# Performance work log

Measured on AMD Instinct MI355X. Metric: run time of the kernel, lower is better.

## Reference

```python
import jax, jax.numpy as jnp
import numpy as np

K = 3
PAD = 1


def _deform_conv(x, offset, weight, bias):
    """torchvision-style deform_conv2d (v1, no mask), stride=1, pad=1, dil=1.
    x: [B,C,H,W], offset: [B,2*K*K,H,W] ordered (dy,dx) per kernel pos (row-major).
    """
    B, C, H, W = x.shape
    K2 = K * K
    off = offset.reshape(B, K2, 2, H, W)
    dy, dx = off[:, :, 0], off[:, :, 1]
    ky = jnp.repeat(jnp.arange(K), K).astype(x.dtype)  # [K2] kernel row offsets
    kx = jnp.tile(jnp.arange(K), K).astype(x.dtype)    # [K2] kernel col offsets
    hh = jnp.arange(H, dtype=x.dtype)
    ww = jnp.arange(W, dtype=x.dtype)
    # sampling positions: [B,K2,H,W]
    py = hh[None, None, :, None] + ky[None, :, None, None] - PAD + dy
    px = ww[None, None, None, :] + kx[None, :, None, None] - PAD + dx
    y0f = jnp.floor(py)
    x0f = jnp.floor(px)
    wy = py - y0f
    wx = px - x0f
    y0 = y0f.astype(jnp.int32)
    x0 = x0f.astype(jnp.int32)
    xf = x.reshape(B, C, H * W)

    def corner(iy, ix, w):
        # zero padding outside the image: contribution masked to 0
        valid = (iy >= 0) & (iy < H) & (ix >= 0) & (ix < W)
        iyc = jnp.clip(iy, 0, H - 1)
        ixc = jnp.clip(ix, 0, W - 1)
        lin = (iyc * W + ixc).reshape(B, -1)                      # [B,K2*H*W]
        g = jnp.take_along_axis(xf, lin[:, None, :], axis=2)     # [B,C,K2*H*W]
        g = g.reshape(B, C, K2, H, W)
        wv = (w * valid.astype(x.dtype))[:, None]                # [B,1,K2,H,W]
        return g * wv

    val = (corner(y0, x0, (1 - wy) * (1 - wx))
           + corner(y0, x0 + 1, (1 - wy) * wx)
           + corner(y0 + 1, x0, wy * (1 - wx))
           + corner(y0 + 1, x0 + 1, wy * wx))                    # [B,C,K2,H,W]
    O = weight.shape[0]
    out = jnp.einsum('ock,bckhw->bohw', weight.reshape(O, C, K2), val)
    return out + bias[None, :, None, None]


def setup_inputs() -> dict:
    key = jax.random.key(0)
    k1, k2, k3, k4, k5 = jax.random.split(key, 5)
    B, C, O, H, W = 4, 64, 64, 128, 128
    fan = C * K * K
    x = jax.random.normal(k1, (B, C, H, W), dtype=jnp.float32)
    w_off = jax.random.normal(k2, (2 * K * K, C, K, K), dtype=jnp.float32) / np.sqrt(fan)
    b_off = jax.random.normal(k3, (2 * K * K,), dtype=jnp.float32) * 0.01
    w_dcn = jax.random.normal(k4, (O, C, K, K), dtype=jnp.float32) / np.sqrt(fan)
    b_dcn = jax.random.normal(k5, (O,), dtype=jnp.float32) * 0.01
    return {"x": x, "w_off": w_off, "b_off": b_off, "w_dcn": w_dcn, "b_dcn": b_dcn}


def reference(x, w_off, b_off, w_dcn, b_dcn):
    offset = jax.lax.conv_general_dilated(
        x, w_off, window_strides=(1, 1), padding=((PAD, PAD), (PAD, PAD)),
        dimension_numbers=('NCHW', 'OIHW', 'NCHW')) + b_off[None, :, None, None]
    return _deform_conv(x, offset, w_dcn, b_dcn)
```

## Files before the change

kernel.cpp:

```cpp
#include <hip/hip_runtime.h>
#include <hip/hip_fp16.h>

#define HH 128
#define WW 128
#define CC 64
#define OO 64
#define HWSZ (HH*WW)

typedef _Float16 f16x8 __attribute__((ext_vector_type(8)));
typedef float    f32x4 __attribute__((ext_vector_type(4)));

__device__ __forceinline__ unsigned short f2h(float f) {
    return __half_as_ushort(__float2half_rn(f));
}

__global__ __launch_bounds__(256) void prep_all(const float* __restrict__ x,
                                                const float* __restrict__ wd,
                                                const float* __restrict__ wo,
                                                unsigned short* __restrict__ xh,
                                                unsigned short* __restrict__ wdtf,
                                                unsigned short* __restrict__ wotf) {
    int t = threadIdx.x;
    if (blockIdx.z == 4) {
        int i = (blockIdx.y * 2 + blockIdx.x) * 256 + t;
        if (i < 36864) {
            int j = i & 7, l = (i >> 3) & 63, nt = (i >> 9) & 3, kcb = i >> 11;
            int k = kcb >> 1, cb = kcb & 1;
            int o = nt * 16 + (l & 15);
            int c = cb * 32 + ((l >> 4) & 3) * 8 + j;
            wdtf[i] = f2h(wd[(o * 64 + c) * 9 + k]);
        } else if (i < 36864 + 18432) {
            int jdx = i - 36864;
            int j = jdx & 7, l = (jdx >> 3) & 63, nt = (jdx >> 9) & 1, kcb = jdx >> 10;
            int k = kcb >> 1, cb = kcb & 1;
            int oc = nt * 16 + (l & 15);
            int c = cb * 32 + ((l >> 4) & 3) * 8 + j;
            wotf[jdx] = f2h(oc < 18 ? wo[(oc * 64 + c) * 9 + k] : 0.0f);
        }
        return;
    }
    __shared__ float tile[64 * 65];
    int w0 = blockIdx.x * 64, h = blockIdx.y, b = blockIdx.z;
    const float* xb = x + ((long)b * CC * HWSZ) + h * WW + w0;
#pragma unroll
    for (int i = 0; i < 16; ++i) {
        int idx = i * 256 + t; int c = idx >> 6, w = idx & 63;
        tile[c * 65 + w] = xb[c * HWSZ + w];
    }
    __syncthreads();
    unsigned short* xo = xh + ((long)((b * HH + h) * WW + w0)) * CC;
#pragma unroll
    for (int i = 0; i < 8; ++i) {
        int idx = i * 256 + t; int w = idx >> 5, c = (idx & 31) * 2;
        ushort2 u;
        u.x = f2h(tile[c * 65 + w]);
        u.y = f2h(tile[(c + 1) * 65 + w]);
        *(ushort2*)(xo + w * CC + c) = u;
    }
}

__global__ __launch_bounds__(256, 2) void fused_dcn(const unsigned short* __restrict__ xh,
                                                    const unsigned short* __restrict__ wotf,
                                                    const float* __restrict__ b_off,
                                                    const unsigned short* __restrict__ wdtf,
                                                    const float* __restrict__ b_dcn,
                                                    float* __restrict__ out) {
    __shared__ __attribute__((aligned(16))) unsigned short shm[32 * 584];
    __shared__ float offs[64 * 20];
    unsigned short* xr    = shm;
    unsigned short* val_s = shm;

    int w0 = blockIdx.x * 64, h = blockIdx.y, b = blockIdx.z;
    int t = threadIdx.x;
    int l = t & 63, wv = t >> 6;
    int m = l & 15, q = l >> 4;

#pragma unroll
    for (int i = 0; i < 7; ++i) {
        int idx = i * 256 + t;
        if (idx < 1584) {
            int r = idx / 528;
            int rem = idx - r * 528;
            int p = rem >> 3, cc = rem & 7;
            int y = h + r - 1, wx = w0 - 1 + p;
            uint4 v = make_uint4(0u, 0u, 0u, 0u);
            if (((unsigned)y < HH) && ((unsigned)wx < WW))
                v = *(const uint4*)(xh + ((long)((b * HH + y) * WW + wx)) * CC + cc * 8);
            *(uint4*)&xr[(r * 68 + p) * 72 + cc * 8] = v;
        }
    }
    __syncthreads();
    {
        int px0 = wv * 16;
        f32x4 acc0 = {0.f, 0.f, 0.f, 0.f}, acc1 = {0.f, 0.f, 0.f, 0.f};
#pragma unroll
        for (int k = 0; k < 9; ++k) {
            int ky = k / 3, kx = k - ky * 3;
            const unsigned short* ar = &xr[(ky * 68 + px0 + m + kx) * 72 + q * 8];
            f16x8 a0 = *(const f16x8*)(ar);
            f16x8 a1 = *(const f16x8*)(ar + 32);
            const unsigned short* bk = wotf + (k * 2) * 2 * 512 + l * 8;
            f16x8 b00 = *(const f16x8*)(bk);
            f16x8 b01 = *(const f16x8*)(bk + 512);
            f16x8 b10 = *(const f16x8*)(bk + 1024);
            f16x8 b11 = *(const f16x8*)(bk + 1536);
            acc0 = __builtin_amdgcn_mfma_f32_16x16x32_f16(a0, b00, acc0, 0, 0, 0);
            acc0 = __builtin_amdgcn_mfma_f32_16x16x32_f16(a1, b10, acc0, 0, 0, 0);
            acc1 = __builtin_amdgcn_mfma_f32_16x16x32_f16(a0, b01, acc1, 0, 0, 0);
            acc1 = __builtin_amdgcn_mfma_f32_16x16x32_f16(a1, b11, acc1, 0, 0, 0);
        }
        float bo0 = b_off[m];
#pragma unroll
        for (int r = 0; r < 4; ++r)
            offs[(px0 + q * 4 + r) * 20 + m] = acc0[r] + bo0;
        if (m < 2) {
            float bo1 = b_off[16 + m];
#pragma unroll
            for (int r = 0; r < 4; ++r)
                offs[(px0 + q * 4 + r) * 20 + 16 + m] = acc1[r] + bo1;
        }
    }
    __syncthreads();

    int spx = t >> 3, ch8 = t & 7;

    f16x8 Breg[18];
#pragma unroll
    for (int kc = 0; kc < 18; ++kc)
        Breg[kc] = *(const f16x8*)(wdtf + (kc * 4 + wv) * 512 + l * 8);

    const unsigned short* xb = xh + (long)b * HWSZ * CC;
    int o = wv * 16 + m;
    float bo = b_dcn[o];
    float* outo = out + ((long)(b * OO + o)) * HWSZ + h * WW;

#pragma unroll
    for (int g = 0; g < 2; ++g) {
        int wg0 = w0 + g * 32;
        const float* oprow = &offs[(g * 32 + spx) * 20];

#pragma unroll
        for (int k = 0; k < 9; ++k) {
            int ky = k / 3, kx = k - ky * 3;
            float2 ov = *(const float2*)(oprow + 2 * k);
            float py  = (float)(h + ky - 1) + ov.x;
            float pxf = (float)(wg0 + spx + kx - 1) + ov.y;
            float y0f = floorf(py), x0f = floorf(pxf);
            float wy = py - y0f, wx = pxf - x0f;
            int y0 = (int)y0f, x0 = (int)x0f, y1 = y0 + 1, x1 = x0 + 1;
            bool vy0 = (unsigned)y0 < HH, vy1 = (unsigned)y1 < HH;
            bool vx0 = (unsigned)x0 < WW, vx1 = (unsigned)x1 < WW;
            int y0c = min(max(y0, 0), HH - 1), y1c = min(max(y1, 0), HH - 1);
            int x0c = min(max(x0, 0), WW - 1), x1c = min(max(x1, 0), WW - 1);
            _Float16 h0 = (_Float16)((vy0 && vx0) ? (1.f - wy) * (1.f - wx) : 0.f);
            _Float16 h1 = (_Float16)((vy0 && vx1) ? (1.f - wy) * wx : 0.f);
            _Float16 h2 = (_Float16)((vy1 && vx0) ? wy * (1.f - wx) : 0.f);
            _Float16 h3 = (_Float16)((vy1 && vx1) ? wy * wx : 0.f);
            f16x8 s00 = *(const f16x8*)(xb + (y0c * WW + x0c) * CC + ch8 * 8);
            f16x8 s01 = *(const f16x8*)(xb + (y0c * WW + x1c) * CC + ch8 * 8);
            f16x8 s10 = *(const f16x8*)(xb + (y1c * WW + x0c) * CC + ch8 * 8);
            f16x8 s11 = *(const f16x8*)(xb + (y1c * WW + x1c) * CC + ch8 * 8);
            f16x8 a = s00 * h0 + s01 * h1 + s10 * h2 + s11 * h3;
            *(f16x8*)&val_s[spx * 584 + k * 64 + ch8 * 8] = a;
        }
        __syncthreads();

        f32x4 acc0 = {0.f, 0.f, 0.f, 0.f}, acc1 = {0.f, 0.f, 0.f, 0.f};
#pragma unroll
        for (int kc = 0; kc < 18; ++kc) {
            f16x8 a0 = *(const f16x8*)&val_s[m * 584 + kc * 32 + q * 8];
            f16x8 a1 = *(const f16x8*)&val_s[(16 + m) * 584 + kc * 32 + q * 8];
            acc0 = __builtin_amdgcn_mfma_f32_16x16x32_f16(a0, Breg[kc], acc0, 0, 0, 0);
            acc1 = __builtin_amdgcn_mfma_f32_16x16x32_f16(a1, Breg[kc], acc1, 0, 0, 0);
        }

        f32x4 r0 = acc0, r1 = acc1;
        r0[0] += bo; r0[1] += bo; r0[2] += bo; r0[3] += bo;
        r1[0] += bo; r1[1] += bo; r1[2] += bo; r1[3] += bo;
        *(f32x4*)(outo + wg0 + q * 4) = r0;
        *(f32x4*)(outo + wg0 + 16 + q * 4) = r1;
        __syncthreads();
    }
}

extern "C" void kernel_launch(void* const* d_in, const int* in_sizes, int n_in,
                              void* d_out, int out_size, void* d_ws, size_t ws_size,
                              hipStream_t stream) {
    const float* x     = (const float*)d_in[0];
    const float* w_off = (const float*)d_in[1];
    const float* b_off = (const float*)d_in[2];
    const float* w_dcn = (const float*)d_in[3];
    const float* b_dcn = (const float*)d_in[4];
    float* out = (float*)d_out;

    char* ws = (char*)d_ws;
    unsigned short* xh   = (unsigned short*)ws;
    unsigned short* wdtf = (unsigned short*)(ws + 8388608);
    unsigned short* wotf = (unsigned short*)(ws + 8462336);

    hipLaunchKernelGGL(prep_all, dim3(2, 128, 5), dim3(256), 0, stream,
                       x, w_dcn, w_off, xh, wdtf, wotf);
    hipLaunchKernelGGL(fused_dcn, dim3(2, 128, 4), dim3(256), 0, stream,
                       xh, wotf, b_off, wdtf, b_dcn, out);
}
```

Baseline: 104.9 us.

## Process two output rows per block to reuse halo tile and weight registers

Each fused block now handles two image rows instead of one. It loads a 4-row halo tile (instead of 3) for the offset conv and computes offsets for both rows. The deformable sampling plus MFMA GEMM stage loops over 4 sub-tiles, so the Breg weight loads and the setup are amortized over twice the work. The change halves the grid, lowers halo reload overhead and raises the occupancy hint to 3, at the cost of more LDS per block and fewer blocks.

```diff
diff --git a/kernel.cpp b/kernel.cpp
--- a/kernel.cpp
+++ b/kernel.cpp
@@ -59,70 +59,72 @@
     }
 }
 
-__global__ __launch_bounds__(256, 2) void fused_dcn(const unsigned short* __restrict__ xh,
+__global__ __launch_bounds__(256, 3) void fused_dcn(const unsigned short* __restrict__ xh,
                                                     const unsigned short* __restrict__ wotf,
                                                     const float* __restrict__ b_off,
                                                     const unsigned short* __restrict__ wdtf,
                                                     const float* __restrict__ b_dcn,
                                                     float* __restrict__ out) {
-    __shared__ __attribute__((aligned(16))) unsigned short shm[32 * 584];
-    __shared__ float offs[64 * 20];
+    __shared__ __attribute__((aligned(16))) unsigned short shm[4 * 68 * 72];
+    __shared__ float offs[128 * 20];
     unsigned short* xr    = shm;
     unsigned short* val_s = shm;
 
-    int w0 = blockIdx.x * 64, h = blockIdx.y, b = blockIdx.z;
+    int w0 = blockIdx.x * 64, h0 = blockIdx.y * 2, b = blockIdx.z;
     int t = threadIdx.x;
     int l = t & 63, wv = t >> 6;
     int m = l & 15, q = l >> 4;
 
 #pragma unroll
-    for (int i = 0; i < 7; ++i) {
+    for (int i = 0; i < 9; ++i) {
         int idx = i * 256 + t;
-        if (idx < 1584) {
-            int r = idx / 528;
-            int rem = idx - r * 528;
+        if (idx < 2112) {
+            int r4 = idx / 528;
+            int rem = idx - r4 * 528;
             int p = rem >> 3, cc = rem & 7;
-            int y = h + r - 1, wx = w0 - 1 + p;
+            int y = h0 + r4 - 1, wx = w0 - 1 + p;
             uint4 v = make_uint4(0u, 0u, 0u, 0u);
             if (((unsigned)y < HH) && ((unsigned)wx < WW))
                 v = *(const uint4*)(xh + ((long)((b * HH + y) * WW + wx)) * CC + cc * 8);
-            *(uint4*)&xr[(r * 68 + p) * 72 + cc * 8] = v;
+            *(uint4*)&xr[(r4 * 68 + p) * 72 + cc * 8] = v;
         }
     }
     __syncthreads();
+
     {
         int px0 = wv * 16;
-        f32x4 acc0 = {0.f, 0.f, 0.f, 0.f}, acc1 = {0.f, 0.f, 0.f, 0.f};
-#pragma unroll
-        for (int k = 0; k < 9; ++k) {
-            int ky = k / 3, kx = k - ky * 3;
-            const unsigned short* ar = &xr[(ky * 68 + px0 + m + kx) * 72 + q * 8];
-            f16x8 a0 = *(const f16x8*)(ar);
-            f16x8 a1 = *(const f16x8*)(ar + 32);
-            const unsigned short* bk = wotf + (k * 2) * 2 * 512 + l * 8;
-            f16x8 b00 = *(const f16x8*)(bk);
-            f16x8 b01 = *(const f16x8*)(bk + 512);
-            f16x8 b10 = *(const f16x8*)(bk + 1024);
-            f16x8 b11 = *(const f16x8*)(bk + 1536);
-            acc0 = __builtin_amdgcn_mfma_f32_16x16x32_f16(a0, b00, acc0, 0, 0, 0);
-            acc0 = __builtin_amdgcn_mfma_f32_16x16x32_f16(a1, b10, acc0, 0, 0, 0);
-            acc1 = __builtin_amdgcn_mfma_f32_16x16x32_f16(a0, b01, acc1, 0, 0, 0);
-            acc1 = __builtin_amdgcn_mfma_f32_16x16x32_f16(a1, b11, acc1, 0, 0, 0);
-        }
         float bo0 = b_off[m];
-#pragma unroll
-        for (int r = 0; r < 4; ++r)
-            offs[(px0 + q * 4 + r) * 20 + m] = acc0[r] + bo0;
-        if (m < 2) {
-            float bo1 = b_off[16 + m];
-#pragma unroll
-            for (int r = 0; r < 4; ++r)
-                offs[(px0 + q * 4 + r) * 20 + 16 + m] = acc1[r] + bo1;
+        float bo1 = (m < 2) ? b_off[16 + m] : 0.0f;
+#pragma unroll
+        for (int r = 0; r < 2; ++r) {
+            f32x4 acc0 = {0.f, 0.f, 0.f, 0.f}, acc1 = {0.f, 0.f, 0.f, 0.f};
+#pragma unroll
+            for (int k = 0; k < 9; ++k) {
+                int ky = k / 3, kx = k - ky * 3;
+                const unsigned short* ar = &xr[((r + ky) * 68 + px0 + m + kx) * 72 + q * 8];
+                f16x8 a0 = *(const f16x8*)(ar);
+                f16x8 a1 = *(const f16x8*)(ar + 32);
+                const unsigned short* bk = wotf + (k * 2) * 2 * 512 + l * 8;
+                f16x8 b00 = *(const f16x8*)(bk);
+                f16x8 b01 = *(const f16x8*)(bk + 512);
+                f16x8 b10 = *(const f16x8*)(bk + 1024);
+                f16x8 b11 = *(const f16x8*)(bk + 1536);
+                acc0 = __builtin_amdgcn_mfma_f32_16x16x32_f16(a0, b00, acc0, 0, 0, 0);
+                acc0 = __builtin_amdgcn_mfma_f32_16x16x32_f16(a1, b10, acc0, 0, 0, 0);
+                acc1 = __builtin_amdgcn_mfma_f32_16x16x32_f16(a0, b01, acc1, 0, 0, 0);
+                acc1 = __builtin_amdgcn_mfma_f32_16x16x32_f16(a1, b11, acc1, 0, 0, 0);
+            }
+#pragma unroll
+            for (int rw = 0; rw < 4; ++rw)
+                offs[(r * 64 + px0 + q * 4 + rw) * 20 + m] = acc0[rw] + bo0;
+            if (m < 2) {
+#pragma unroll
+                for (int rw = 0; rw < 4; ++rw)
+                    offs[(r * 64 + px0 + q * 4 + rw) * 20 + 16 + m] = acc1[rw] + bo1;
+            }
         }
     }
     __syncthreads();
-
-    int spx = t >> 3, ch8 = t & 7;
 
     f16x8 Breg[18];
 #pragma unroll
@@ -130,20 +132,22 @@
         Breg[kc] = *(const f16x8*)(wdtf + (kc * 4 + wv) * 512 + l * 8);
 
     const unsigned short* xb = xh + (long)b * HWSZ * CC;
+    int spx = t >> 3, ch8 = (t & 7) * 8;
     int o = wv * 16 + m;
     float bo = b_dcn[o];
-    float* outo = out + ((long)(b * OO + o)) * HWSZ + h * WW;
-
-#pragma unroll
-    for (int g = 0; g < 2; ++g) {
+
+#pragma unroll
+    for (int st = 0; st < 4; ++st) {
+        int r = st >> 1, g = st & 1;
+        int hrow = h0 + r;
         int wg0 = w0 + g * 32;
-        const float* oprow = &offs[(g * 32 + spx) * 20];
+        const float* oprow = &offs[(r * 64 + g * 32 + spx) * 20];
 
 #pragma unroll
         for (int k = 0; k < 9; ++k) {
             int ky = k / 3, kx = k - ky * 3;
             float2 ov = *(const float2*)(oprow + 2 * k);
-            float py  = (float)(h + ky - 1) + ov.x;
+            float py  = (float)(hrow + ky - 1) + ov.x;
             float pxf = (float)(wg0 + spx + kx - 1) + ov.y;
             float y0f = floorf(py), x0f = floorf(pxf);
             float wy = py - y0f, wx = pxf - x0f;
@@ -152,16 +156,16 @@
             bool vx0 = (unsigned)x0 < WW, vx1 = (unsigned)x1 < WW;
             int y0c = min(max(y0, 0), HH - 1), y1c = min(max(y1, 0), HH - 1);
             int x0c = min(max(x0, 0), WW - 1), x1c = min(max(x1, 0), WW - 1);
-            _Float16 h0 = (_Float16)((vy0 && vx0) ? (1.f - wy) * (1.f - wx) : 0.f);
-            _Float16 h1 = (_Float16)((vy0 && vx1) ? (1.f - wy) * wx : 0.f);
-            _Float16 h2 = (_Float16)((vy1 && vx0) ? wy * (1.f - wx) : 0.f);
-            _Float16 h3 = (_Float16)((vy1 && vx1) ? wy * wx : 0.f);
-            f16x8 s00 = *(const f16x8*)(xb + (y0c * WW + x0c) * CC + ch8 * 8);
-            f16x8 s01 = *(const f16x8*)(xb + (y0c * WW + x1c) * CC + ch8 * 8);
-            f16x8 s10 = *(const f16x8*)(xb + (y1c * WW + x0c) * CC + ch8 * 8);
-            f16x8 s11 = *(const f16x8*)(xb + (y1c * WW + x1c) * CC + ch8 * 8);
-            f16x8 a = s00 * h0 + s01 * h1 + s10 * h2 + s11 * h3;
-            *(f16x8*)&val_s[spx * 584 + k * 64 + ch8 * 8] = a;
+            _Float16 h0w = (_Float16)((vy0 && vx0) ? (1.f - wy) * (1.f - wx) : 0.f);
+            _Float16 h1w = (_Float16)((vy0 && vx1) ? (1.f - wy) * wx : 0.f);
+            _Float16 h2w = (_Float16)((vy1 && vx0) ? wy * (1.f - wx) : 0.f);
+            _Float16 h3w = (_Float16)((vy1 && vx1) ? wy * wx : 0.f);
+            f16x8 s00 = *(const f16x8*)(xb + (y0c * WW + x0c) * CC + ch8);
+            f16x8 s01 = *(const f16x8*)(xb + (y0c * WW + x1c) * CC + ch8);
+            f16x8 s10 = *(const f16x8*)(xb + (y1c * WW + x0c) * CC + ch8);
+            f16x8 s11 = *(const f16x8*)(xb + (y1c * WW + x1c) * CC + ch8);
+            f16x8 a = s00 * h0w + s01 * h1w + s10 * h2w + s11 * h3w;
+            *(f16x8*)&val_s[spx * 584 + k * 64 + ch8] = a;
         }
         __syncthreads();
 
@@ -174,12 +178,13 @@
             acc1 = __builtin_amdgcn_mfma_f32_16x16x32_f16(a1, Breg[kc], acc1, 0, 0, 0);
         }
 
+        float* outo = out + ((long)(b * OO + o) * HH + hrow) * WW + wg0;
         f32x4 r0 = acc0, r1 = acc1;
         r0[0] += bo; r0[1] += bo; r0[2] += bo; r0[3] += bo;
         r1[0] += bo; r1[1] += bo; r1[2] += bo; r1[3] += bo;
-        *(f32x4*)(outo + wg0 + q * 4) = r0;
-        *(f32x4*)(outo + wg0 + 16 + q * 4) = r1;
-        __syncthreads();
+        *(f32x4*)(outo + q * 4) = r0;
+        *(f32x4*)(outo + 16 + q * 4) = r1;
+        if (st < 3) __syncthreads();
     }
 }
 
@@ -200,6 +205,6 @@
 
     hipLaunchKernelGGL(prep_all, dim3(2, 128, 5), dim3(256), 0, stream,
                        x, w_dcn, w_off, xh, wdtf, wotf);
-    hipLaunchKernelGGL(fused_dcn, dim3(2, 128, 4), dim3(256), 0, stream,
+    hipLaunchKernelGGL(fused_dcn, dim3(2, 64, 4), dim3(256), 0, stream,
                        xh, wotf, b_off, wdtf, b_dcn, out);
 }
```

Measured after the change: 105.1 us. No clear change (+0.2%).

## Swizzle block order for XCD-local rows, raise occupancy bound, drop final barrier

Applied to the files above, without the earlier changes.

Launches a 1D grid and remaps block IDs so that consecutive blocks scheduled on the same XCD (id mod 8) cover contiguous row bands of one image. This keeps the neighbouring rows used for gathers in that XCD's L2. It also raises the launch-bounds occupancy hint from 2 to 3 blocks per SIMD, which constrains registers and may spill the 18 Breg vectors. The trailing __syncthreads after the last group is removed, and the channel offset is now precomputed.

```diff
diff --git a/kernel.cpp b/kernel.cpp
--- a/kernel.cpp
+++ b/kernel.cpp
@@ -59,7 +59,7 @@
     }
 }
 
-__global__ __launch_bounds__(256, 2) void fused_dcn(const unsigned short* __restrict__ xh,
+__global__ __launch_bounds__(256, 3) void fused_dcn(const unsigned short* __restrict__ xh,
                                                     const unsigned short* __restrict__ wotf,
                                                     const float* __restrict__ b_off,
                                                     const unsigned short* __restrict__ wdtf,
@@ -70,7 +70,15 @@
     unsigned short* xr    = shm;
     unsigned short* val_s = shm;
 
-    int w0 = blockIdx.x * 64, h = blockIdx.y, b = blockIdx.z;
+    int id = blockIdx.x;
+    int c8 = id & 7;
+    int j  = id >> 3;
+    int g  = (j >> 5) * 8 + c8;
+    int inner = j & 31;
+    int b  = g >> 3;
+    int h  = (g & 7) * 16 + (inner >> 1);
+    int w0 = (inner & 1) * 64;
+
     int t = threadIdx.x;
     int l = t & 63, wv = t >> 6;
     int m = l & 15, q = l >> 4;
@@ -122,7 +130,7 @@
     }
     __syncthreads();
 
-    int spx = t >> 3, ch8 = t & 7;
+    int spx = t >> 3, ch8 = (t & 7) * 8;
 
     f16x8 Breg[18];
 #pragma unroll
@@ -135,9 +143,9 @@
     float* outo = out + ((long)(b * OO + o)) * HWSZ + h * WW;
 
 #pragma unroll
-    for (int g = 0; g < 2; ++g) {
-        int wg0 = w0 + g * 32;
-        const float* oprow = &offs[(g * 32 + spx) * 20];
+    for (int g2 = 0; g2 < 2; ++g2) {
+        int wg0 = w0 + g2 * 32;
+        const float* oprow = &offs[(g2 * 32 + spx) * 20];
 
 #pragma unroll
         for (int k = 0; k < 9; ++k) {
@@ -152,16 +160,16 @@
             bool vx0 = (unsigned)x0 < WW, vx1 = (unsigned)x1 < WW;
             int y0c = min(max(y0, 0), HH - 1), y1c = min(max(y1, 0), HH - 1);
             int x0c = min(max(x0, 0), WW - 1), x1c = min(max(x1, 0), WW - 1);
-            _Float16 h0 = (_Float16)((vy0 && vx0) ? (1.f - wy) * (1.f - wx) : 0.f);
-            _Float16 h1 = (_Float16)((vy0 && vx1) ? (1.f - wy) * wx : 0.f);
-            _Float16 h2 = (_Float16)((vy1 && vx0) ? wy * (1.f - wx) : 0.f);
-            _Float16 h3 = (_Float16)((vy1 && vx1) ? wy * wx : 0.f);
-            f16x8 s00 = *(const f16x8*)(xb + (y0c * WW + x0c) * CC + ch8 * 8);
-            f16x8 s01 = *(const f16x8*)(xb + (y0c * WW + x1c) * CC + ch8 * 8);
-            f16x8 s10 = *(const f16x8*)(xb + (y1c * WW + x0c) * CC + ch8 * 8);
-            f16x8 s11 = *(const f16x8*)(xb + (y1c * WW + x1c) * CC + ch8 * 8);
-            f16x8 a = s00 * h0 + s01 * h1 + s10 * h2 + s11 * h3;
-            *(f16x8*)&val_s[spx * 584 + k * 64 + ch8 * 8] = a;
+            _Float16 h0w = (_Float16)((vy0 && vx0) ? (1.f - wy) * (1.f - wx) : 0.f);
+            _Float16 h1w = (_Float16)((vy0 && vx1) ? (1.f - wy) * wx : 0.f);
+            _Float16 h2w = (_Float16)((vy1 && vx0) ? wy * (1.f - wx) : 0.f);
+            _Float16 h3w = (_Float16)((vy1 && vx1) ? wy * wx : 0.f);
+            f16x8 s00 = *(const f16x8*)(xb + (y0c * WW + x0c) * CC + ch8);
+            f16x8 s01 = *(const f16x8*)(xb + (y0c * WW + x1c) * CC + ch8);
+            f16x8 s10 = *(const f16x8*)(xb + (y1c * WW + x0c) * CC + ch8);
+            f16x8 s11 = *(const f16x8*)(xb + (y1c * WW + x1c) * CC + ch8);
+            f16x8 a = s00 * h0w + s01 * h1w + s10 * h2w + s11 * h3w;
+            *(f16x8*)&val_s[spx * 584 + k * 64 + ch8] = a;
         }
         __syncthreads();
 
@@ -179,7 +187,7 @@
         r1[0] += bo; r1[1] += bo; r1[2] += bo; r1[3] += bo;
         *(f32x4*)(outo + wg0 + q * 4) = r0;
         *(f32x4*)(outo + wg0 + 16 + q * 4) = r1;
-        __syncthreads();
+        if (g2 == 0) __syncthreads();
     }
 }
 
@@ -200,6 +208,6 @@
 
     hipLaunchKernelGGL(prep_all, dim3(2, 128, 5), dim3(256), 0, stream,
                        x, w_dcn, w_off, xh, wdtf, wotf);
-    hipLaunchKernelGGL(fused_dcn, dim3(2, 128, 4), dim3(256), 0, stream,
+    hipLaunchKernelGGL(fused_dcn, dim3(1024), dim3(256), 0, stream,
                        xh, wotf, b_off, wdtf, b_dcn, out);
 }
```

Result: no change. 103.5 us (-1.3%).
